# Kernel optimization log

Measured on AMD Instinct MI355X. Metric: run time of the kernel, lower is better.

## Reference

```python
import jax, jax.numpy as jnp
import numpy as np

B, S, D = 2, 1024, 1024
H, KV, HD = 16, 4, 64
E, K, F = 8, 2, 2048
EPS = 1e-6
THETA = 10000.0
LAYER = 0


def setup_inputs() -> dict:
    key = jax.random.key(0)
    ks = jax.random.split(key, 12)
    sc = 0.02
    return {
        "hidden_states": jax.random.normal(ks[0], (B, S, D), jnp.float32),
        "position_ids": jnp.broadcast_to(jnp.arange(S, dtype=jnp.int32), (B, S)),
        "gate_scores": jnp.zeros((1, B, S, E), jnp.float32),
        "ln1_w": jnp.ones((D,), jnp.float32),
        "ln2_w": jnp.ones((D,), jnp.float32),
        "wq": jax.random.normal(ks[1], (D, H * HD), jnp.float32) * sc,
        "wk": jax.random.normal(ks[2], (D, KV * HD), jnp.float32) * sc,
        "wv": jax.random.normal(ks[3], (D, KV * HD), jnp.float32) * sc,
        "wo": jax.random.normal(ks[4], (H * HD, D), jnp.float32) * sc,
        "gate_w": jax.random.normal(ks[5], (D, E), jnp.float32) * sc,
        "w1": jax.random.normal(ks[6], (E, D, F), jnp.float32) * sc,
        "w3": jax.random.normal(ks[7], (E, D, F), jnp.float32) * sc,
        "w2": jax.random.normal(ks[8], (E, F, D), jnp.float32) * sc,
    }


def rms_norm(x, w):
    var = jnp.mean(jnp.square(x), axis=-1, keepdims=True)
    return x * jax.lax.rsqrt(var + EPS) * w


def rotate_half(x):
    x1, x2 = jnp.split(x, 2, axis=-1)
    return jnp.concatenate([-x2, x1], axis=-1)


def apply_rope(q, k, position_ids):
    inv_freq = 1.0 / (THETA ** (jnp.arange(0, HD, 2, dtype=jnp.float32) / HD))
    freqs = position_ids.astype(jnp.float32)[..., None] * inv_freq  # [B,S,HD/2]
    emb = jnp.concatenate([freqs, freqs], axis=-1)  # [B,S,HD]
    cos = jnp.cos(emb)[:, :, None, :]
    sin = jnp.sin(emb)[:, :, None, :]
    q = q * cos + rotate_half(q) * sin
    k = k * cos + rotate_half(k) * sin
    return q, k


def attention(x, position_ids, wq, wk, wv, wo):
    q = (x @ wq).reshape(B, S, H, HD)
    k = (x @ wk).reshape(B, S, KV, HD)
    v = (x @ wv).reshape(B, S, KV, HD)
    q, k = apply_rope(q, k, position_ids)
    rep = H // KV
    k = jnp.repeat(k, rep, axis=2)  # [B,S,H,HD]
    v = jnp.repeat(v, rep, axis=2)
    scores = jnp.einsum("bqhd,bkhd->bhqk", q, k) / jnp.sqrt(jnp.float32(HD))
    causal = jnp.tril(jnp.ones((S, S), bool))
    scores = jnp.where(causal, scores, jnp.finfo(scores.dtype).min)
    p = jax.nn.softmax(scores, axis=-1)
    out = jnp.einsum("bhqk,bkhd->bqhd", p, v).reshape(B, S, H * HD)
    return out @ wo


def moe(x, gate_w, w1, w3, w2):
    xt = x.reshape(-1, D)  # [T,D]
    router_logits = xt @ gate_w  # [T,E]
    routing_weights = jax.nn.softmax(router_logits.astype(jnp.float32), axis=-1)
    routing_scores = routing_weights.reshape(B, S, E)
    top_w, top_e = jax.lax.top_k(routing_weights, K)  # [T,K]
    top_w = top_w / jnp.sum(top_w, axis=-1, keepdims=True)
    top_w = top_w.astype(xt.dtype)
    # combined per-(token,expert) weight; zero when not routed
    comb = jnp.sum(jax.nn.one_hot(top_e, E, dtype=xt.dtype) * top_w[..., None], axis=1)  # [T,E]
    # SwiGLU experts, dense-dispatch formulation (same math as gather/scatter)
    h = jax.nn.silu(jnp.einsum("td,edf->etf", xt, w1)) * jnp.einsum("td,edf->etf", xt, w3)
    y = jnp.einsum("etf,efd->etd", h, w2)  # [E,T,D]
    out = jnp.einsum("etd,te->td", y, comb)
    return out.reshape(B, S, D), routing_scores


def reference(hidden_states, position_ids, gate_scores, ln1_w, ln2_w, wq, wk, wv, wo, gate_w, w1, w3, w2):
    residual = hidden_states
    h = rms_norm(hidden_states, ln1_w)
    h = residual + attention(h, position_ids, wq, wk, wv, wo)
    residual = h
    hn = rms_norm(h, ln2_w)
    moe_out, routing_scores = moe(hn, gate_w, w1, w3, w2)
    h = residual + moe_out
    gate_scores = gate_scores.at[LAYER].set(routing_scores)
    return h, gate_scores
```

## Files before the change

kernel.cpp:

```cpp
#include <hip/hip_runtime.h>
#include <hip/hip_bf16.h>
#include <stdint.h>

using bf16 = __hip_bfloat16;
using bf16x8 = __attribute__((ext_vector_type(8))) __bf16;
using f32x4  = __attribute__((ext_vector_type(4))) float;

#define NTOK 2048
#define DIM 1024
#define NH 16
#define NKV 4
#define HDIM 64
#define NE 8
#define NF 2048
#define SEQ 1024
#define MAXR 5120
#define MAXTILES 40

__device__ __forceinline__ float b2f(unsigned short u){ unsigned v=((unsigned)u)<<16; float f; __builtin_memcpy(&f,&v,4); return f; }
__device__ __forceinline__ unsigned short f2b(float f){ bf16 h=__float2bfloat16(f); unsigned short u; __builtin_memcpy(&u,&h,2); return u; }

typedef __attribute__((address_space(3))) unsigned int lds_u32;
typedef const __attribute__((address_space(1))) unsigned int glb_u32;
__device__ __forceinline__ void lds16(const void* g, void* l){
  __builtin_amdgcn_global_load_lds((glb_u32*)g, (lds_u32*)l, 16, 0, 0);
}

__global__ void k_zero_i32(int* p, int n){ int i=blockIdx.x*256+threadIdx.x; if(i<n) p[i]=0; }

__global__ __launch_bounds__(256) void k_transpose(const float* __restrict__ in, bf16* __restrict__ out,
    int R, int C, size_t inz, size_t outz){
  __shared__ float tile[32][33];
  int bx = blockIdx.x*32, by = blockIdx.y*32;
  const float* src = in + (size_t)blockIdx.z * inz;
  bf16* dst = out + (size_t)blockIdx.z * outz;
  int x = threadIdx.x, y0 = threadIdx.y;
#pragma unroll
  for (int i=0;i<4;i++){ int r = y0 + i*8; tile[r][x] = src[(size_t)(by+r)*C + bx + x]; }
  __syncthreads();
#pragma unroll
  for (int i=0;i<4;i++){ int c = y0 + i*8; dst[(size_t)(bx+c)*R + by + x] = __float2bfloat16(tile[x][c]); }
}

__global__ __launch_bounds__(256) void k_tbf(const bf16* __restrict__ in, bf16* __restrict__ out, int R, int C){
  __shared__ unsigned short tile[32][33];
  int bx = blockIdx.x*32, by = blockIdx.y*32;
  size_t base = (size_t)blockIdx.z * R * C;
  const unsigned short* src = (const unsigned short*)in + base;
  unsigned short* dst = (unsigned short*)out + base;
  int x = threadIdx.x, y0 = threadIdx.y;
#pragma unroll
  for (int i=0;i<4;i++){ int r = y0 + i*8; tile[r][x] = src[(size_t)(by+r)*C + bx + x]; }
  __syncthreads();
#pragma unroll
  for (int i=0;i<4;i++){ int c = y0 + i*8; dst[(size_t)(bx+c)*R + by + x] = tile[x][c]; }
}

__global__ __launch_bounds__(256) void k_rmsnorm(const float* __restrict__ x, const float* __restrict__ w, bf16* __restrict__ out){
  int row = blockIdx.x, t = threadIdx.x;
  const float4 v = ((const float4*)(x + (size_t)row*DIM))[t];
  float ss = v.x*v.x + v.y*v.y + v.z*v.z + v.w*v.w;
#pragma unroll
  for (int m=1;m<64;m<<=1) ss += __shfl_xor(ss, m);
  __shared__ float red[4];
  if ((t&63)==0) red[t>>6] = ss;
  __syncthreads();
  float tot = red[0]+red[1]+red[2]+red[3];
  float r = rsqrtf(tot * (1.0f/DIM) + 1e-6f);
  const float4 wv = ((const float4*)w)[t];
  ushort4 o;
  o.x = f2b(v.x*r*wv.x); o.y = f2b(v.y*r*wv.y); o.z = f2b(v.z*r*wv.z); o.w = f2b(v.w*r*wv.w);
  ((ushort4*)(out + (size_t)row*DIM))[t] = o;
}

#define BM 128
#define BN 128
#define BK 32

template<int MODE>
__global__ __launch_bounds__(256) void k_gemm(
    const bf16* __restrict__ A, const bf16* __restrict__ Bt,
    bf16* __restrict__ Cb, float* __restrict__ Cf, const float* __restrict__ resid,
    const int* __restrict__ tile_expert, const int* __restrict__ row_tok,
    const float* __restrict__ row_w, const int* __restrict__ row_slot,
    int N, int K)
{
  int tn = blockIdx.x, tm = blockIdx.y;
  int e = 0;
  if constexpr (MODE >= 2){ e = tile_expert[tm]; if (e < 0) return; }
  const bf16* Ablk = A + (size_t)tm*BM*K;
  const bf16* Bblk = Bt + ((MODE>=2) ? (size_t)e*N*K : (size_t)0) + (size_t)tn*BN*K;

  __shared__ bf16 lA[BM*BK];
  __shared__ bf16 lB[BN*BK];

  int t = threadIdx.x;
  int lane = t & 63, wave = t >> 6;
  int wr = wave >> 1, wc = wave & 1;
  int lr = lane & 15, lg = lane >> 4;

  int srow = wave*32 + (lane >> 2);
  int scol = (lane & 3) * 8;

  f32x4 acc[4][4] = {};

  for (int k0 = 0; k0 < K; k0 += BK){
    __syncthreads();
    lds16(Ablk + (size_t)srow*K        + k0 + scol, lA + wave*1024);
    lds16(Ablk + (size_t)(srow+16)*K   + k0 + scol, lA + wave*1024 + 512);
    lds16(Bblk + (size_t)srow*K        + k0 + scol, lB + wave*1024);
    lds16(Bblk + (size_t)(srow+16)*K   + k0 + scol, lB + wave*1024 + 512);
    __syncthreads();
    bf16x8 af[4], bfv[4];
#pragma unroll
    for (int m=0;m<4;m++) af[m]  = *(const bf16x8*)(lA + (wr*64 + m*16 + lr)*BK + lg*8);
#pragma unroll
    for (int n=0;n<4;n++) bfv[n] = *(const bf16x8*)(lB + (wc*64 + n*16 + lr)*BK + lg*8);
#pragma unroll
    for (int m=0;m<4;m++)
#pragma unroll
      for (int n=0;n<4;n++)
        acc[m][n] = __builtin_amdgcn_mfma_f32_16x16x32_bf16(af[m], bfv[n], acc[m][n], 0, 0, 0);
  }

#pragma unroll
  for (int m=0;m<4;m++){
#pragma unroll
    for (int n=0;n<4;n++){
      int col = tn*BN + wc*64 + n*16 + lr;
#pragma unroll
      for (int j=0;j<4;j++){
        int row = tm*BM + wr*64 + m*16 + lg*4 + j;
        float v = acc[m][n][j];
        if constexpr (MODE==0 || MODE==2){
          Cb[(size_t)row*N + col] = __float2bfloat16(v);
        } else if constexpr (MODE==1){
          Cf[(size_t)row*N + col] = v + resid[(size_t)row*N + col];
        } else {
          int tok = row_tok[row];
          if (tok >= 0) Cf[((size_t)row_slot[row]*NTOK + tok)*DIM + col] = v * row_w[row];
        }
      }
    }
  }
}

__global__ __launch_bounds__(64) void k_rope(const bf16* __restrict__ qkv, const int* __restrict__ pos_ids,
    bf16* __restrict__ qr, bf16* __restrict__ kr, bf16* __restrict__ vr){
  int tk = blockIdx.x;
  int b = tk >> 10, s = tk & 1023;
  int d = threadIdx.x;
  float p = (float)pos_ids[tk];
  int i = d & 31;
  float freq = p * powf(10000.0f, -(float)(2*i)*(1.0f/HDIM));
  float sn, cs;
  sincosf(freq, &sn, &cs);
  const bf16* row = qkv + (size_t)tk*1536;
#pragma unroll
  for (int h=0; h<NH; h++){
    float x  = __bfloat162float(row[h*64 + d]);
    float xp = __bfloat162float(row[h*64 + ((d+32)&63)]);
    float rh = (d<32) ? -xp : xp;
    qr[(((size_t)(b*NH+h)*SEQ)+s)*HDIM + d] = __float2bfloat16(x*cs + rh*sn);
  }
#pragma unroll
  for (int h=0; h<NKV; h++){
    float x  = __bfloat162float(row[1024 + h*64 + d]);
    float xp = __bfloat162float(row[1024 + h*64 + ((d+32)&63)]);
    float rh = (d<32) ? -xp : xp;
    kr[(((size_t)(b*NKV+h)*SEQ)+s)*HDIM + d] = __float2bfloat16(x*cs + rh*sn);
    vr[(((size_t)(b*NKV+h)*SEQ)+s)*HDIM + d] = row[1280 + h*64 + d];
  }
}

__global__ __launch_bounds__(64) void k_attn_mfma(const bf16* __restrict__ qr, const bf16* __restrict__ kr,
    const bf16* __restrict__ vT, bf16* __restrict__ out){
  int qt = blockIdx.x, h = blockIdx.y, b = blockIdx.z;
  int lane = threadIdx.x;
  int g = lane >> 4, c = lane & 15;
  int kv = h >> 2;
  int qbase = qt*16;
  const bf16* Qb = qr + (((size_t)(b*NH+h)*SEQ) + qbase)*HDIM;
  const bf16* Kb = kr + ((size_t)(b*NKV+kv)*SEQ)*HDIM;
  const bf16* Vt = vT + ((size_t)(b*NKV+kv)*HDIM)*SEQ;

  bf16x8 qa[2];
  qa[0] = *(const bf16x8*)(Qb + (size_t)c*HDIM + g*8);
  qa[1] = *(const bf16x8*)(Qb + (size_t)c*HDIM + 32 + g*8);

  f32x4 acc[4] = {};
  float m[4], l[4];
#pragma unroll
  for (int j=0;j<4;j++){ m[j] = -1e30f; l[j] = 0.f; }

  __shared__ bf16 P[16][40];

  int kend = qbase + 15;
  for (int k0 = 0; k0 <= kend; k0 += 32){
    f32x4 s[2] = {};
#pragma unroll
    for (int cn=0;cn<2;cn++){
#pragma unroll
      for (int dk=0;dk<2;dk++){
        bf16x8 kb = *(const bf16x8*)(Kb + (size_t)(k0+cn*16+c)*HDIM + dk*32 + g*8);
        s[cn] = __builtin_amdgcn_mfma_f32_16x16x32_bf16(qa[dk], kb, s[cn], 0, 0, 0);
      }
    }
    float sv[2][4];
    bool boundary = (k0 + 31 > qbase);
#pragma unroll
    for (int cn=0;cn<2;cn++){
#pragma unroll
      for (int j=0;j<4;j++){
        float v = s[cn][j] * 0.125f;
        if (boundary){
          int cg = k0 + cn*16 + c, rg = qbase + g*4 + j;
          if (cg > rg) v = -1e30f;
        }
        sv[cn][j] = v;
      }
    }
#pragma unroll
    for (int j=0;j<4;j++){
      float rmax = fmaxf(sv[0][j], sv[1][j]);
#pragma unroll
      for (int mk=1;mk<16;mk<<=1) rmax = fmaxf(rmax, __shfl_xor(rmax, mk));
      float mn = fmaxf(m[j], rmax);
      float corr = __expf(m[j] - mn);
      m[j] = mn;
      float p0 = __expf(sv[0][j] - mn);
      float p1 = __expf(sv[1][j] - mn);
      float rs = p0 + p1;
#pragma unroll
      for (int mk=1;mk<16;mk<<=1) rs += __shfl_xor(rs, mk);
      l[j] = l[j]*corr + rs;
#pragma unroll
      for (int db=0;db<4;db++) acc[db][j] *= corr;
      P[g*4+j][c]      = __float2bfloat16(p0);
      P[g*4+j][16+c]   = __float2bfloat16(p1);
    }
    __syncthreads();
    bf16x8 pa = *(const bf16x8*)(&P[c][g*8]);
#pragma unroll
    for (int db=0;db<4;db++){
      bf16x8 vb = *(const bf16x8*)(Vt + (size_t)(db*16+c)*SEQ + k0 + g*8);
      acc[db] = __builtin_amdgcn_mfma_f32_16x16x32_bf16(pa, vb, acc[db], 0, 0, 0);
    }
    __syncthreads();
  }
#pragma unroll
  for (int j=0;j<4;j++){
    float inv = 1.f / l[j];
    size_t rowoff = (size_t)(b*SEQ + qbase + g*4 + j)*1024 + h*64;
#pragma unroll
    for (int db=0;db<4;db++)
      out[rowoff + db*16 + c] = __float2bfloat16(acc[db][j] * inv);
  }
}

__global__ __launch_bounds__(64) void k_router(const float* __restrict__ h1, const float* __restrict__ ln2w,
    const float* __restrict__ gw, float* __restrict__ scores,
    int* __restrict__ top_e, float* __restrict__ top_w, int* __restrict__ cnt){
  int tk = blockIdx.x, lane = threadIdx.x;
  const float* xr = h1 + (size_t)tk*DIM;
  const float4* x4 = (const float4*)xr;
  float4 xv[4];
  float ss = 0.f;
#pragma unroll
  for (int i=0;i<4;i++){
    xv[i] = x4[lane*4+i];
    ss += xv[i].x*xv[i].x + xv[i].y*xv[i].y + xv[i].z*xv[i].z + xv[i].w*xv[i].w;
  }
#pragma unroll
  for (int mm=1;mm<64;mm<<=1) ss += __shfl_xor(ss, mm);
  float r = rsqrtf(ss*(1.0f/DIM) + 1e-6f);
  float acc[8] = {0,0,0,0,0,0,0,0};
#pragma unroll
  for (int i=0;i<16;i++){
    int d = lane*16 + i;
    float xd = ((const float*)xv)[i];
    float xn = xd * r * ln2w[d];
    const float* g = gw + (size_t)d*NE;
#pragma unroll
    for (int e=0;e<8;e++) acc[e] += xn * g[e];
  }
#pragma unroll
  for (int e=0;e<8;e++){
#pragma unroll
    for (int mm=1;mm<64;mm<<=1) acc[e] += __shfl_xor(acc[e], mm);
  }
  float mx = acc[0];
#pragma unroll
  for (int e=1;e<8;e++) mx = fmaxf(mx, acc[e]);
  float w[8]; float se = 0.f;
#pragma unroll
  for (int e=0;e<8;e++){ w[e] = expf(acc[e]-mx); se += w[e]; }
  float inv = 1.f/se;
#pragma unroll
  for (int e=0;e<8;e++) w[e] *= inv;
  if (lane < 8) scores[(size_t)tk*NE + lane] = w[lane];
  if (lane == 0){
    int e1=0; float m1=w[0];
#pragma unroll
    for (int i=1;i<8;i++) if (w[i] > m1){ m1=w[i]; e1=i; }
    int e2=-1; float m2=-1.f;
#pragma unroll
    for (int i=0;i<8;i++) if (i!=e1 && w[i] > m2){ m2=w[i]; e2=i; }
    float s12 = m1 + m2;
    top_e[2*tk] = e1;   top_w[2*tk]   = m1/s12;
    top_e[2*tk+1] = e2; top_w[2*tk+1] = m2/s12;
    atomicAdd(&cnt[e1], 1); atomicAdd(&cnt[e2], 1);
  }
}

__global__ __launch_bounds__(256) void k_offsets(const int* __restrict__ cnt, int* __restrict__ seg_off,
    int* __restrict__ tile_expert, int* __restrict__ row_tok){
  int t = threadIdx.x;
  for (int i=t;i<MAXR;i+=256) row_tok[i] = -1;
  for (int i=t;i<MAXTILES;i+=256) tile_expert[i] = -1;
  __syncthreads();
  if (t == 0){
    int off = 0;
    for (int e=0;e<NE;e++){
      seg_off[e] = off;
      int nt = (cnt[e] + 127) >> 7;
      for (int i=0;i<nt;i++) tile_expert[(off>>7)+i] = e;
      off += nt << 7;
    }
  }
}

__global__ __launch_bounds__(256) void k_scatter(const int* __restrict__ top_e, const float* __restrict__ top_w,
    const int* __restrict__ seg_off, int* __restrict__ cnt2,
    int* __restrict__ row_tok, float* __restrict__ row_w, int* __restrict__ row_slot){
  int tkn = blockIdx.x*256 + threadIdx.x;
  if (tkn >= NTOK) return;
#pragma unroll
  for (int k=0;k<2;k++){
    int e = top_e[2*tkn+k];
    int p = atomicAdd(&cnt2[e], 1);
    int r = seg_off[e] + p;
    row_tok[r] = tkn; row_w[r] = top_w[2*tkn+k]; row_slot[r] = k;
  }
}

__global__ __launch_bounds__(256) void k_gather(const int* __restrict__ row_tok, const bf16* __restrict__ xn,
    bf16* __restrict__ Xg){
  int r = blockIdx.x, t = threadIdx.x;
  int tok = row_tok[r];
  ushort4* dst = (ushort4*)(Xg + (size_t)r*DIM) + t;
  if (tok < 0){ ushort4 z; z.x=0; z.y=0; z.z=0; z.w=0; *dst = z; }
  else *dst = ((const ushort4*)(xn + (size_t)tok*DIM))[t];
}

__global__ __launch_bounds__(256) void k_silumul(const bf16* __restrict__ h13, bf16* __restrict__ o){
  size_t i = (size_t)blockIdx.x*256 + threadIdx.x;
  size_t r = i >> 9;
  int fq = (int)(i & 511);
  const bf16* rowp = h13 + r*(2*NF);
  ushort4 ua = ((const ushort4*)rowp)[fq];
  ushort4 ub = ((const ushort4*)(rowp + NF))[fq];
  ushort4 uo;
  { float fa=b2f(ua.x), fb=b2f(ub.x); uo.x = f2b(fa/(1.f+__expf(-fa))*fb); }
  { float fa=b2f(ua.y), fb=b2f(ub.y); uo.y = f2b(fa/(1.f+__expf(-fa))*fb); }
  { float fa=b2f(ua.z), fb=b2f(ub.z); uo.z = f2b(fa/(1.f+__expf(-fa))*fb); }
  { float fa=b2f(ua.w), fb=b2f(ub.w); uo.w = f2b(fa/(1.f+__expf(-fa))*fb); }
  ((ushort4*)(o))[i] = uo;
}

__global__ __launch_bounds__(256) void k_final(const float* __restrict__ h1, const float* __restrict__ ybuf, float* __restrict__ out){
  size_t i = (size_t)blockIdx.x*256 + threadIdx.x;
  float4 a  = ((const float4*)h1)[i];
  float4 b0 = ((const float4*)ybuf)[i];
  float4 b1 = ((const float4*)(ybuf + (size_t)NTOK*DIM))[i];
  float4 r;
  r.x = a.x+b0.x+b1.x; r.y = a.y+b0.y+b1.y; r.z = a.z+b0.z+b1.z; r.w = a.w+b0.w+b1.w;
  ((float4*)out)[i] = r;
}

extern "C" void kernel_launch(void* const* d_in, const int* in_sizes, int n_in,
                              void* d_out, int out_size, void* d_ws, size_t ws_size,
                              hipStream_t stream){
  const float* hidden = (const float*)d_in[0];
  const int*   pos    = (const int*)d_in[1];
  const float* ln1    = (const float*)d_in[3];
  const float* ln2    = (const float*)d_in[4];
  const float* wq     = (const float*)d_in[5];
  const float* wk     = (const float*)d_in[6];
  const float* wv     = (const float*)d_in[7];
  const float* wo     = (const float*)d_in[8];
  const float* gw     = (const float*)d_in[9];
  const float* w1     = (const float*)d_in[10];
  const float* w3     = (const float*)d_in[11];
  const float* w2     = (const float*)d_in[12];
  float* out1 = (float*)d_out;
  float* out2 = out1 + (size_t)NTOK*DIM;

  char* p = (char*)d_ws;
  auto take = [&](size_t bytes){ void* r = (void*)p; p += (bytes + 255) & ~(size_t)255; return r; };
  bf16* wqkvT = (bf16*)take((size_t)1536*1024*2);
  bf16* woT   = (bf16*)take((size_t)1024*1024*2);
  bf16* w13T  = (bf16*)take((size_t)NE*2*NF*DIM*2);
  bf16* w2T   = (bf16*)take((size_t)NE*DIM*NF*2);
  float* h1   = (float*)take((size_t)NTOK*DIM*4);
  bf16* xn2   = (bf16*)take((size_t)NTOK*DIM*2);
  int*  cnt   = (int*)take(64);
  int*  cnt2  = cnt + 8;
  int*  seg_off     = (int*)take(64);
  int*  tile_expert = (int*)take(MAXTILES*4);
  int*  top_e  = (int*)take((size_t)NTOK*2*4);
  float* top_w = (float*)take((size_t)NTOK*2*4);
  int*  row_tok  = (int*)take((size_t)MAXR*4);
  float* row_w   = (float*)take((size_t)MAXR*4);
  int*  row_slot = (int*)take((size_t)MAXR*4);
  bf16* Xg     = (bf16*)take((size_t)MAXR*DIM*2);
  bf16* h13buf = (bf16*)take((size_t)MAXR*2*NF*2);
  bf16* hbuf   = (bf16*)take((size_t)MAXR*NF*2);
  char* ra = (char*)Xg;
  bf16* xn1 = (bf16*)ra;       ra += (size_t)NTOK*DIM*2;
  bf16* qkv = (bf16*)ra;       ra += (size_t)NTOK*1536*2;
  bf16* qr  = (bf16*)ra;       ra += (size_t)NTOK*DIM*2;
  bf16* krp = (bf16*)ra;       ra += (size_t)NTOK*NKV*HDIM*2;
  bf16* vrp = (bf16*)ra;       ra += (size_t)NTOK*NKV*HDIM*2;
  bf16* vTp = (bf16*)ra;       ra += (size_t)NTOK*NKV*HDIM*2;
  bf16* attn_out = (bf16*)ra;  ra += (size_t)NTOK*DIM*2;
  float* ybuf = (float*)h13buf;

  k_zero_i32<<<dim3(1), dim3(256), 0, stream>>>(cnt, 16);
  k_transpose<<<dim3(32,32,1), dim3(32,8), 0, stream>>>(wq, wqkvT, 1024, 1024, (size_t)1024*1024, (size_t)1024*1024);
  k_transpose<<<dim3(8,32,1),  dim3(32,8), 0, stream>>>(wk, wqkvT + (size_t)1024*1024, 1024, 256, (size_t)1024*256, (size_t)1024*256);
  k_transpose<<<dim3(8,32,1),  dim3(32,8), 0, stream>>>(wv, wqkvT + (size_t)1280*1024, 1024, 256, (size_t)1024*256, (size_t)1024*256);
  k_transpose<<<dim3(32,32,1), dim3(32,8), 0, stream>>>(wo, woT, 1024, 1024, (size_t)1024*1024, (size_t)1024*1024);
  k_transpose<<<dim3(NF/32, DIM/32, NE), dim3(32,8), 0, stream>>>(w1, w13T, DIM, NF, (size_t)DIM*NF, (size_t)2*NF*DIM);
  k_transpose<<<dim3(NF/32, DIM/32, NE), dim3(32,8), 0, stream>>>(w3, w13T + (size_t)NF*DIM, DIM, NF, (size_t)DIM*NF, (size_t)2*NF*DIM);
  k_transpose<<<dim3(DIM/32, NF/32, NE), dim3(32,8), 0, stream>>>(w2, w2T, NF, DIM, (size_t)NF*DIM, (size_t)NF*DIM);
  k_rmsnorm<<<dim3(NTOK), dim3(256), 0, stream>>>(hidden, ln1, xn1);
  k_gemm<0><<<dim3(1536/BN, NTOK/BM), dim3(256), 0, stream>>>(xn1, wqkvT, qkv, nullptr, nullptr, nullptr, nullptr, nullptr, nullptr, 1536, 1024);
  k_rope<<<dim3(NTOK), dim3(64), 0, stream>>>(qkv, pos, qr, krp, vrp);
  k_tbf<<<dim3(HDIM/32, SEQ/32, 2*NKV), dim3(32,8), 0, stream>>>(vrp, vTp, SEQ, HDIM);
  k_attn_mfma<<<dim3(SEQ/16, NH, 2), dim3(64), 0, stream>>>(qr, krp, vTp, attn_out);
  k_gemm<1><<<dim3(DIM/BN, NTOK/BM), dim3(256), 0, stream>>>(attn_out, woT, nullptr, h1, hidden, nullptr, nullptr, nullptr, nullptr, DIM, 1024);
  k_rmsnorm<<<dim3(NTOK), dim3(256), 0, stream>>>(h1, ln2, xn2);
  k_router<<<dim3(NTOK), dim3(64), 0, stream>>>(h1, ln2, gw, out2, top_e, top_w, cnt);
  k_offsets<<<dim3(1), dim3(256), 0, stream>>>(cnt, seg_off, tile_expert, row_tok);
  k_scatter<<<dim3(NTOK/256), dim3(256), 0, stream>>>(top_e, top_w, seg_off, cnt2, row_tok, row_w, row_slot);
  k_gather<<<dim3(MAXR), dim3(256), 0, stream>>>(row_tok, xn2, Xg);
  k_gemm<2><<<dim3(2*NF/BN, MAXTILES), dim3(256), 0, stream>>>(Xg, w13T, h13buf, nullptr, nullptr, tile_expert, nullptr, nullptr, nullptr, 2*NF, DIM);
  k_silumul<<<dim3((unsigned)((size_t)MAXR*NF/4/256)), dim3(256), 0, stream>>>(h13buf, hbuf);
  k_gemm<3><<<dim3(DIM/BN, MAXTILES), dim3(256), 0, stream>>>(hbuf, w2T, nullptr, ybuf, nullptr, tile_expert, row_tok, row_w, row_slot, DIM, NF);
  k_final<<<dim3(NTOK*DIM/4/256), dim3(256), 0, stream>>>(h1, ybuf, out1);
}
```

Baseline: 617.0 us.

## Retile GEMM with BK=64, XOR-swizzled LDS, templated BM, fuse rmsnorm into router

```diff
diff --git a/kernel.cpp b/kernel.cpp
--- a/kernel.cpp
+++ b/kernel.cpp
@@ -73,11 +73,10 @@
   ((ushort4*)(out + (size_t)row*DIM))[t] = o;
 }
 
-#define BM 128
 #define BN 128
-#define BK 32
-
-template<int MODE>
+#define BK 64
+
+template<int MODE, int BMT>
 __global__ __launch_bounds__(256) void k_gemm(
     const bf16* __restrict__ A, const bf16* __restrict__ Bt,
     bf16* __restrict__ Cb, float* __restrict__ Cf, const float* __restrict__ resid,
@@ -87,11 +86,11 @@
 {
   int tn = blockIdx.x, tm = blockIdx.y;
   int e = 0;
-  if constexpr (MODE >= 2){ e = tile_expert[tm]; if (e < 0) return; }
-  const bf16* Ablk = A + (size_t)tm*BM*K;
+  if constexpr (MODE >= 2){ e = tile_expert[(tm*BMT)>>7]; if (e < 0) return; }
+  const bf16* Ablk = A + (size_t)tm*BMT*K;
   const bf16* Bblk = Bt + ((MODE>=2) ? (size_t)e*N*K : (size_t)0) + (size_t)tn*BN*K;
 
-  __shared__ bf16 lA[BM*BK];
+  __shared__ bf16 lA[BMT*BK];
   __shared__ bf16 lB[BN*BK];
 
   int t = threadIdx.x;
@@ -99,38 +98,55 @@
   int wr = wave >> 1, wc = wave & 1;
   int lr = lane & 15, lg = lane >> 4;
 
-  int srow = wave*32 + (lane >> 2);
-  int scol = (lane & 3) * 8;
-
-  f32x4 acc[4][4] = {};
+  int sln  = lane >> 3;
+  int scol = ((lane & 7) ^ sln) * 8;
+  constexpr int AR = BMT/4;
+  int sArow = wave*AR + sln;
+  int sBrow = wave*32 + sln;
+
+  constexpr int MF = BMT/32;
+  f32x4 acc[MF][4] = {};
+
+  int swz = lr & 7;
 
   for (int k0 = 0; k0 < K; k0 += BK){
     __syncthreads();
-    lds16(Ablk + (size_t)srow*K        + k0 + scol, lA + wave*1024);
-    lds16(Ablk + (size_t)(srow+16)*K   + k0 + scol, lA + wave*1024 + 512);
-    lds16(Bblk + (size_t)srow*K        + k0 + scol, lB + wave*1024);
-    lds16(Bblk + (size_t)(srow+16)*K   + k0 + scol, lB + wave*1024 + 512);
+#pragma unroll
+    for (int ch = 0; ch < AR/8; ch++)
+      lds16(Ablk + (size_t)(sArow + ch*8)*K + k0 + scol, lA + (wave*AR + ch*8)*BK);
+#pragma unroll
+    for (int ch = 0; ch < 4; ch++)
+      lds16(Bblk + (size_t)(sBrow + ch*8)*K + k0 + scol, lB + (wave*32 + ch*8)*BK);
     __syncthreads();
-    bf16x8 af[4], bfv[4];
-#pragma unroll
-    for (int m=0;m<4;m++) af[m]  = *(const bf16x8*)(lA + (wr*64 + m*16 + lr)*BK + lg*8);
-#pragma unroll
-    for (int n=0;n<4;n++) bfv[n] = *(const bf16x8*)(lB + (wc*64 + n*16 + lr)*BK + lg*8);
-#pragma unroll
-    for (int m=0;m<4;m++)
-#pragma unroll
-      for (int n=0;n<4;n++)
-        acc[m][n] = __builtin_amdgcn_mfma_f32_16x16x32_bf16(af[m], bfv[n], acc[m][n], 0, 0, 0);
-  }
-
-#pragma unroll
-  for (int m=0;m<4;m++){
+#pragma unroll
+    for (int kk = 0; kk < 2; kk++){
+      bf16x8 af[MF], bfv[4];
+#pragma unroll
+      for (int m=0;m<MF;m++){
+        int R = wr*(BMT/2) + m*16 + lr;
+        af[m] = *(const bf16x8*)(lA + R*BK + ((((kk<<2)|lg) ^ swz)<<3));
+      }
+#pragma unroll
+      for (int n=0;n<4;n++){
+        int R = wc*64 + n*16 + lr;
+        bfv[n] = *(const bf16x8*)(lB + R*BK + ((((kk<<2)|lg) ^ swz)<<3));
+      }
+#pragma unroll
+      for (int m=0;m<MF;m++)
+#pragma unroll
+        for (int n=0;n<4;n++)
+          acc[m][n] = __builtin_amdgcn_mfma_f32_16x16x32_bf16(af[m], bfv[n], acc[m][n], 0, 0, 0);
+    }
+  }
+
+#pragma unroll
+  for (int m=0;m<MF;m++){
 #pragma unroll
     for (int n=0;n<4;n++){
       int col = tn*BN + wc*64 + n*16 + lr;
 #pragma unroll
       for (int j=0;j<4;j++){
-        int row = tm*BM + wr*64 + m*16 + lg*4 + j;
+        int row = tm*BMT + wr*(BMT/2) + m*16 + lg*4 + j;
         float v = acc[m][n][j];
         if constexpr (MODE==0 || MODE==2){
           Cb[(size_t)row*N + col] = __float2bfloat16(v);
@@ -259,7 +275,7 @@
 }
 
 __global__ __launch_bounds__(64) void k_router(const float* __restrict__ h1, const float* __restrict__ ln2w,
-    const float* __restrict__ gw, float* __restrict__ scores,
+    const float* __restrict__ gw, float* __restrict__ scores, bf16* __restrict__ xn2,
     int* __restrict__ top_e, float* __restrict__ top_w, int* __restrict__ cnt){
   int tk = blockIdx.x, lane = threadIdx.x;
   const float* xr = h1 + (size_t)tk*DIM;
@@ -275,15 +291,20 @@
   for (int mm=1;mm<64;mm<<=1) ss += __shfl_xor(ss, mm);
   float r = rsqrtf(ss*(1.0f/DIM) + 1e-6f);
   float acc[8] = {0,0,0,0,0,0,0,0};
+  unsigned short xo[16];
 #pragma unroll
   for (int i=0;i<16;i++){
     int d = lane*16 + i;
     float xd = ((const float*)xv)[i];
     float xn = xd * r * ln2w[d];
+    xo[i] = f2b(xn);
     const float* g = gw + (size_t)d*NE;
 #pragma unroll
     for (int e=0;e<8;e++) acc[e] += xn * g[e];
   }
+#pragma unroll
+  for (int i=0;i<4;i++)
+    ((ushort4*)(xn2 + (size_t)tk*DIM + lane*16))[i] = *(ushort4*)(xo + i*4);
 #pragma unroll
   for (int e=0;e<8;e++){
 #pragma unroll
@@ -435,18 +456,17 @@
   k_transpose<<<dim3(NF/32, DIM/32, NE), dim3(32,8), 0, stream>>>(w3, w13T + (size_t)NF*DIM, DIM, NF, (size_t)DIM*NF, (size_t)2*NF*DIM);
   k_transpose<<<dim3(DIM/32, NF/32, NE), dim3(32,8), 0, stream>>>(w2, w2T, NF, DIM, (size_t)NF*DIM, (size_t)NF*DIM);
   k_rmsnorm<<<dim3(NTOK), dim3(256), 0, stream>>>(hidden, ln1, xn1);
-  k_gemm<0><<<dim3(1536/BN, NTOK/BM), dim3(256), 0, stream>>>(xn1, wqkvT, qkv, nullptr, nullptr, nullptr, nullptr, nullptr, nullptr, 1536, 1024);
+  k_gemm<0,64><<<dim3(1536/BN, NTOK/64), dim3(256), 0, stream>>>(xn1, wqkvT, qkv, nullptr, nullptr, nullptr, nullptr, nullptr, nullptr, 1536, 1024);
   k_rope<<<dim3(NTOK), dim3(64), 0, stream>>>(qkv, pos, qr, krp, vrp);
   k_tbf<<<dim3(HDIM/32, SEQ/32, 2*NKV), dim3(32,8), 0, stream>>>(vrp, vTp, SEQ, HDIM);
   k_attn_mfma<<<dim3(SEQ/16, NH, 2), dim3(64), 0, stream>>>(qr, krp, vTp, attn_out);
-  k_gemm<1><<<dim3(DIM/BN, NTOK/BM), dim3(256), 0, stream>>>(attn_out, woT, nullptr, h1, hidden, nullptr, nullptr, nullptr, nullptr, DIM, 1024);
-  k_rmsnorm<<<dim3(NTOK), dim3(256), 0, stream>>>(h1, ln2, xn2);
-  k_router<<<dim3(NTOK), dim3(64), 0, stream>>>(h1, ln2, gw, out2, top_e, top_w, cnt);
+  k_gemm<1,64><<<dim3(DIM/BN, NTOK/64), dim3(256), 0, stream>>>(attn_out, woT, nullptr, h1, hidden, nullptr, nullptr, nullptr, nullptr, DIM, 1024);
+  k_router<<<dim3(NTOK), dim3(64), 0, stream>>>(h1, ln2, gw, out2, xn2, top_e, top_w, cnt);
   k_offsets<<<dim3(1), dim3(256), 0, stream>>>(cnt, seg_off, tile_expert, row_tok);
   k_scatter<<<dim3(NTOK/256), dim3(256), 0, stream>>>(top_e, top_w, seg_off, cnt2, row_tok, row_w, row_slot);
   k_gather<<<dim3(MAXR), dim3(256), 0, stream>>>(row_tok, xn2, Xg);
-  k_gemm<2><<<dim3(2*NF/BN, MAXTILES), dim3(256), 0, stream>>>(Xg, w13T, h13buf, nullptr, nullptr, tile_expert, nullptr, nullptr, nullptr, 2*NF, DIM);
+  k_gemm<2,128><<<dim3(2*NF/BN, MAXR/128), dim3(256), 0, stream>>>(Xg, w13T, h13buf, nullptr, nullptr, tile_expert, nullptr, nullptr, nullptr, 2*NF, DIM);
   k_silumul<<<dim3((unsigned)((size_t)MAXR*NF/4/256)), dim3(256), 0, stream>>>(h13buf, hbuf);
-  k_gemm<3><<<dim3(DIM/BN, MAXTILES), dim3(256), 0, stream>>>(hbuf, w2T, nullptr, ybuf, nullptr, tile_expert, row_tok, row_w, row_slot, DIM, NF);
+  k_gemm<3,64><<<dim3(DIM/BN, MAXR/64), dim3(256), 0, stream>>>(hbuf, w2T, nullptr, ybuf, nullptr, tile_expert, row_tok, row_w, row_slot, DIM, NF);
   k_final<<<dim3(NTOK*DIM/4/256), dim3(256), 0, stream>>>(h1, ybuf, out1);
 }
```

New measurement: 563.5 us. -8.7%, faster.
